# Optimization experiments

Measured on AMD Instinct MI355X. Metric: run time of the kernel, lower is better.

## Reference

```python
import jax, jax.numpy as jnp
import numpy as np

B, L, IN, H, W = 4096, 10, 8, 512, 512


def setup_inputs() -> dict:
    key = jax.random.key(0)
    ks = jax.random.split(key, 24)
    s = 0.05  # small init so tanh/sigmoid stay in active range
    def rn(k, shape):
        return jax.random.normal(k, shape, dtype=jnp.float32) * s
    return {
        "items": jax.random.normal(ks[0], (B, L, IN), dtype=jnp.float32),
        "decoder_items_input": jax.random.uniform(ks[1], (B, H), dtype=jnp.float32),
        "emb_w": rn(ks[2], (H, IN)), "emb_b": rn(ks[3], (H,)),
        "enc_wih": rn(ks[4], (3 * H, H)), "enc_whh": rn(ks[5], (3 * H, H)),
        "enc_bih": rn(ks[6], (3 * H,)), "enc_bhh": rn(ks[7], (3 * H,)),
        "dec_wih": rn(ks[8], (3 * H, H)), "dec_whh": rn(ks[9], (3 * H, H)),
        "dec_bih": rn(ks[10], (3 * H,)), "dec_bhh": rn(ks[11], (3 * H,)),
        "w1": rn(ks[12], (W, H)), "w2": rn(ks[13], (W, H)),
        "w3": rn(ks[14], (W, H)), "w4": rn(ks[15], (W, H)),
        "w5": rn(ks[16], (W, H)), "w6": rn(ks[17], (W, H)),
        "w7": rn(ks[18], (W, 2 * H)),
        "v1": rn(ks[19], (W,)), "v2": rn(ks[20], (W,)),
        "v3_w": rn(ks[21], (W,)), "v3_b": rn(ks[22], (1,)),
        "wori": rn(ks[23], (6, 3 * H)), "bori": jnp.zeros((6,), jnp.float32),
    }


def _gru_scan(xg, whh, bhh, h0):
    # xg: [L,B,3H] precomputed input-gate projections; returns all hidden states [L,B,H]
    def step(h, xg_t):
        hg = h @ whh.T + bhh
        xr, xz, xn = jnp.split(xg_t, 3, axis=-1)
        hr, hz, hn = jnp.split(hg, 3, axis=-1)
        r = jax.nn.sigmoid(xr + hr)
        z = jax.nn.sigmoid(xz + hz)
        n = jnp.tanh(xn + r * hn)
        h_new = (1.0 - z) * n + z * h
        return h_new, h_new
    _, ys = jax.lax.scan(step, h0, xg)
    return ys


def _forward(items, decoder_items_input, emb_w, emb_b, enc_wih, enc_whh, enc_bih, enc_bhh,
             dec_wih, dec_whh, dec_bih, dec_bhh, w1, w2, w3, w4, w5, w6, w7,
             v1, v2, v3_w, v3_b, wori, bori):
    Bsz, Lln, _ = items.shape
    Hh = emb_w.shape[0]
    x = items @ emb_w.T + emb_b                                  # [B,L,H] embedding
    xg = (x @ enc_wih.T + enc_bih).transpose(1, 0, 2)            # [L,B,3H]
    enc_out = _gru_scan(xg, enc_whh, enc_bhh, jnp.zeros((Bsz, Hh), x.dtype))  # [L,B,H]
    h0 = enc_out[-1]                                             # last encoder state
    enc_blh = enc_out.transpose(1, 0, 2)                         # [B,L,H]
    enc_w3 = enc_out @ w3.T                                      # [L,B,W] (hoisted, step-invariant)
    enc_w6 = enc_out @ w6.T                                      # [L,B,W]
    xg_dec = decoder_items_input @ dec_wih.T + dec_bih           # [B,3H] constant decoder input
    xr, xz, xn = jnp.split(xg_dec, 3, axis=-1)

    def step(h, _):
        hg = h @ dec_whh.T + dec_bhh
        hr, hz, hn = jnp.split(hg, 3, axis=-1)
        r = jax.nn.sigmoid(xr + hr)
        z = jax.nn.sigmoid(xz + hz)
        n = jnp.tanh(xn + r * hn)
        h_new = (1.0 - z) * n + z * h                            # GRUCell update
        # intra attention cache is always length-1 in the source (the shape[1]==1 branch
        # always fires), so log_softmax is over a singleton axis -> exactly zero.
        doi = h_new[:, None, :]                                  # [B,1,H]
        oi = jnp.tanh(h_new @ w1.T + h_new @ w2.T) @ v1          # [B]
        attnd = jax.nn.log_softmax(oi[:, None, None], axis=-1)   # [B,1,1] zeros
        hi = (attnd * doi).sum(axis=1)                           # [B,H] (zeros, faithful)
        sm = jnp.tanh(enc_w3 + h_new @ w4.T + hi @ w5.T)         # [L,B,W]
        out_seq = (sm @ v2).T                                    # [B,L]
        sm_ori = jnp.tanh(enc_w6 + jnp.concatenate([h_new, hi], axis=-1) @ w7.T)  # [L,B,W]
        oo = sm_ori @ v3_w + v3_b[0]                             # [L,B]
        attnc = jax.nn.log_softmax(oo.T[:, :, None], axis=-1)    # [B,L,1] zeros (singleton axis)
        he = (attnc * enc_blh).sum(axis=1)                       # [B,H]
        total = jnp.concatenate([he, h_new, hi], axis=-1)        # [B,3H]
        out_ori = total @ wori.T + bori                          # [B,6]
        return h_new, (out_seq, out_ori)

    _, (seqs, oris) = jax.lax.scan(step, h0, None, length=Lln)
    probs_seq = seqs.transpose(1, 0, 2)                          # [B,L,L]
    probs_ori = oris.transpose(1, 0, 2)                          # [B,L,6]
    return probs_seq, probs_ori


def reference(items, decoder_items_input, emb_w, emb_b, enc_wih, enc_whh, enc_bih, enc_bhh,
              dec_wih, dec_whh, dec_bih, dec_bhh, w1, w2, w3, w4, w5, w6, w7,
              v1, v2, v3_w, v3_b, wori, bori):
    return _forward(items, decoder_items_input, emb_w, emb_b, enc_wih, enc_whh, enc_bih,
                    enc_bhh, dec_wih, dec_whh, dec_bih, dec_bhh, w1, w2, w3, w4, w5, w6,
                    w7, v1, v2, v3_w, v3_b, wori, bori)
```

## Files before the change

kernel.cpp:

```cpp
#include <hip/hip_runtime.h>
#include <hip/hip_bf16.h>


#define B_   4096
#define L_   10
#define IN_  8
#define H_   512
#define H3_  1536
#define W_   512
#define ORI_BASE (B_ * L_ * L_)

typedef __attribute__((ext_vector_type(8))) short s8v;
typedef __attribute__((ext_vector_type(4))) float f4v;

#define LOG2E  1.4426950408889634f
#define LOG2E2 2.8853900817779268f

__device__ __forceinline__ float sig_fast(float x) {
  float e = __builtin_amdgcn_exp2f(-x * LOG2E);
  return __builtin_amdgcn_rcpf(1.f + e);
}
__device__ __forceinline__ float tanh_fast(float x) {
  float e = __builtin_amdgcn_exp2f(x * LOG2E2);
  return 1.f - 2.f * __builtin_amdgcn_rcpf(e + 1.f);
}
__device__ __forceinline__ short f2bf(float f) {
  __hip_bfloat16 h = __float2bfloat16(f);
  return __builtin_bit_cast(short, h);
}
__device__ __forceinline__ float bf2f(short s) {
  __hip_bfloat16 h = __builtin_bit_cast(__hip_bfloat16, s);
  return __bfloat162float(h);
}
__device__ __forceinline__ void stc(float* p, float v) { *p = v; }
__device__ __forceinline__ void stc(short* p, float v) { *p = f2bf(v); }

__global__ __launch_bounds__(256) void f2bf_k(const float* __restrict__ src,
                                              short* __restrict__ dst, int n)
{
  int i = blockIdx.x * 256 + threadIdx.x;
  if (i < n) dst[i] = f2bf(src[i]);
}

__global__ __launch_bounds__(256) void build_wc(
    const float* __restrict__ enc_wih, const float* __restrict__ emb_w,
    const float* __restrict__ emb_b, const float* __restrict__ enc_bih,
    float* __restrict__ Wc, float* __restrict__ bc)
{
  __shared__ float se[H_ * IN_];
  __shared__ float sb[H_];
  const int tid = threadIdx.x;
  for (int i = tid; i < H_ * IN_; i += 256) se[i] = emb_w[i];
  for (int i = tid; i < H_; i += 256) sb[i] = emb_b[i];
  __syncthreads();
  int g = (blockIdx.x * 256 + tid) >> 6;
  int lane = tid & 63;
  const float* wr = enc_wih + (long)g * H_ + lane * 8;
  float w8[8];
#pragma unroll
  for (int j = 0; j < 8; ++j) w8[j] = wr[j];
  float acc[9] = {};
#pragma unroll
  for (int kk = 0; kk < 8; ++kk) {
    int k = lane * 8 + kk;
#pragma unroll
    for (int j = 0; j < 8; ++j) acc[j] += w8[kk] * se[k * IN_ + j];
    acc[8] += w8[kk] * sb[k];
  }
#pragma unroll
  for (int j = 0; j < 9; ++j)
#pragma unroll
    for (int off = 32; off; off >>= 1) acc[j] += __shfl_down(acc[j], off, 64);
  if (lane == 0) {
#pragma unroll
    for (int j = 0; j < 8; ++j) Wc[g * IN_ + j] = acc[j];
    bc[g] = acc[8] + enc_bih[g];
  }
}

template <typename CT>
__global__ __launch_bounds__(256) void gemm_bf16(
    const short* __restrict__ A, long lda,
    const short* __restrict__ Bw, long ldb,
    const float* __restrict__ bias,
    CT* __restrict__ C, long ldc, int K, float scale)
{
  __shared__ short As[128 * 32];
  __shared__ short Bs[128 * 32];
  const int tid = threadIdx.x;
  const long row0 = (long)blockIdx.y * 128;
  const long col0 = (long)blockIdx.x * 128;
  const int wave = tid >> 6, lane = tid & 63;
  const int wm = (wave & 1) * 64, wn = (wave >> 1) * 64;
  const int r16 = lane & 15, quad = lane >> 4;
  f4v acc[4][4] = {};

  for (int k0 = 0; k0 < K; k0 += 32) {
#pragma unroll
    for (int r = 0; r < 2; ++r) {
      int idx = r * 256 + tid;
      int m = idx >> 2;
      int k8 = (idx & 3) * 8;
      __builtin_amdgcn_global_load_lds(
          (const __attribute__((address_space(1))) void*)(A + (row0 + m) * lda + k0 + k8),
          (__attribute__((address_space(3))) void*)(As + idx * 8), 16, 0, 0);
      __builtin_amdgcn_global_load_lds(
          (const __attribute__((address_space(1))) void*)(Bw + (col0 + m) * ldb + k0 + k8),
          (__attribute__((address_space(3))) void*)(Bs + idx * 8), 16, 0, 0);
    }
    __syncthreads();
    s8v af[4], bf[4];
#pragma unroll
    for (int i = 0; i < 4; ++i)
      af[i] = *(const s8v*)&As[(wm + i * 16 + r16) * 32 + quad * 8];
#pragma unroll
    for (int j = 0; j < 4; ++j)
      bf[j] = *(const s8v*)&Bs[(wn + j * 16 + r16) * 32 + quad * 8];
#pragma unroll
    for (int i = 0; i < 4; ++i)
#pragma unroll
      for (int j = 0; j < 4; ++j)
        acc[i][j] = __builtin_amdgcn_mfma_f32_16x16x32_bf16(af[i], bf[j], acc[i][j], 0, 0, 0);
    __syncthreads();
  }

#pragma unroll
  for (int i = 0; i < 4; ++i) {
    long rbase = row0 + wm + i * 16 + quad * 4;
#pragma unroll
    for (int j = 0; j < 4; ++j) {
      long c = col0 + wn + j * 16 + r16;
      float bv = bias ? bias[c] : 0.f;
#pragma unroll
      for (int rg = 0; rg < 4; ++rg)
        stc(&C[(rbase + rg) * ldc + c], (acc[i][j][rg] + bv) * scale);
    }
  }
}

template <bool ENC>
__global__ __launch_bounds__(256) void gru_fused(
    const short* __restrict__ Aprev,
    const short* __restrict__ Whh,
    const float* __restrict__ bhh,
    const short* __restrict__ xg,
    const float* __restrict__ items_t,
    const float* __restrict__ Wc,
    const float* __restrict__ bc,
    float* __restrict__ h,
    short* __restrict__ hout)
{
  __shared__ short As[2][64 * 64];
  __shared__ short Bs[2][192 * 64];
  const int tid = threadIdx.x;
  const long row0 = (long)blockIdx.y * 64;
  const int col0 = blockIdx.x * 64;
  const int wave = tid >> 6, lane = tid & 63;
  const int r16 = lane & 15, quad = lane >> 4;
  const int sw = r16 & 7;

  f4v acc[3][4] = {};

  auto stage = [&](int buf, int k0) {
#pragma unroll
    for (int r = 0; r < 2; ++r) {
      int idx = r * 256 + tid;
      int m = idx >> 3, c8 = idx & 7;
      int src = c8 ^ (m & 7);
      __builtin_amdgcn_global_load_lds(
          (const __attribute__((address_space(1))) void*)(Aprev + (row0 + m) * H_ + k0 + src * 8),
          (__attribute__((address_space(3))) void*)(&As[buf][idx * 8]), 16, 0, 0);
    }
#pragma unroll
    for (int r = 0; r < 6; ++r) {
      int idx = r * 256 + tid;
      int m = idx >> 3, c8 = idx & 7;
      int src = c8 ^ (m & 7);
      int g = m >> 6, cc = m & 63;
      __builtin_amdgcn_global_load_lds(
          (const __attribute__((address_space(1))) void*)(Whh + ((long)g * H_ + col0 + cc) * H_ + k0 + src * 8),
          (__attribute__((address_space(3))) void*)(&Bs[buf][idx * 8]), 16, 0, 0);
    }
  };

  stage(0, 0);
  int cur = 0;
  for (int k = 0; k < 8; ++k) {
    if (k < 7) {
      stage(cur ^ 1, (k + 1) * 64);
      asm volatile("s_waitcnt vmcnt(8)" ::: "memory");
    } else {
      asm volatile("s_waitcnt vmcnt(0)" ::: "memory");
    }
    __builtin_amdgcn_s_barrier();
    s8v af[4][2], bf[3][2];
#pragma unroll
    for (int i = 0; i < 4; ++i)
#pragma unroll
      for (int hh = 0; hh < 2; ++hh)
        af[i][hh] = *(const s8v*)&As[cur][(i * 16 + r16) * 64 + ((hh * 4 + quad) ^ sw) * 8];
#pragma unroll
    for (int g = 0; g < 3; ++g)
#pragma unroll
      for (int hh = 0; hh < 2; ++hh)
        bf[g][hh] = *(const s8v*)&Bs[cur][(g * 64 + wave * 16 + r16) * 64 + ((hh * 4 + quad) ^ sw) * 8];
    __builtin_amdgcn_s_setprio(1);
#pragma unroll
    for (int hh = 0; hh < 2; ++hh)
#pragma unroll
      for (int g = 0; g < 3; ++g)
#pragma unroll
        for (int i = 0; i < 4; ++i)
          acc[g][i] = __builtin_amdgcn_mfma_f32_16x16x32_bf16(af[i][hh], bf[g][hh], acc[g][i], 0, 0, 0);
    __builtin_amdgcn_s_setprio(0);
    __builtin_amdgcn_s_barrier();
    cur ^= 1;
  }

  const int col = col0 + wave * 16 + r16;
  float wc[3][8], bcv[3];
  if (ENC) {
#pragma unroll
    for (int g = 0; g < 3; ++g) {
      const float* wr = Wc + ((long)g * H_ + col) * IN_;
#pragma unroll
      for (int j = 0; j < 8; ++j) wc[g][j] = wr[j];
      bcv[g] = bc[g * H_ + col];
    }
    float* itemS = (float*)As;
    int i2 = tid * 2;
    int m = i2 >> 3, j = i2 & 7;
    itemS[i2] = items_t[(row0 + m) * (L_ * IN_) + j];
    itemS[i2 + 1] = items_t[(row0 + m) * (L_ * IN_) + j + 1];
    __syncthreads();
  }
  float bhr = bhh[col], bhz = bhh[col + H_], bhn = bhh[col + 2 * H_];

#pragma unroll
  for (int i = 0; i < 4; ++i) {
#pragma unroll
    for (int rg = 0; rg < 4; ++rg) {
      int rl = i * 16 + quad * 4 + rg;
      long row = row0 + rl;
      float xr, xz, xn;
      if (ENC) {
        const float* it = (const float*)As + rl * 8;
        xr = bcv[0]; xz = bcv[1]; xn = bcv[2];
#pragma unroll
        for (int j = 0; j < 8; ++j) {
          float iv = it[j];
          xr += iv * wc[0][j];
          xz += iv * wc[1][j];
          xn += iv * wc[2][j];
        }
      } else {
        long gx = row * H3_ + col;
        xr = bf2f(xg[gx]); xz = bf2f(xg[gx + H_]); xn = bf2f(xg[gx + 2 * H_]);
      }
      float r = sig_fast(xr + acc[0][i][rg] + bhr);
      float z = sig_fast(xz + acc[1][i][rg] + bhz);
      float n = tanh_fast(xn + r * (acc[2][i][rg] + bhn));
      long hi = row * H_ + col;
      float hv = (1.f - z) * n + z * h[hi];
      h[hi] = hv;
      hout[hi] = f2bf(hv);
    }
  }
}

__global__ __launch_bounds__(256) void out_seq_all(
    const short* __restrict__ ew3,
    const short* __restrict__ a4,
    const float* __restrict__ v2,
    float* __restrict__ out)
{
  __shared__ float se[L_ * W_];
  __shared__ float sa[L_ * W_];
  const int b = blockIdx.x;
  const int tid = threadIdx.x;
  for (int i = tid; i < L_ * W_ / 8; i += 256) {
    int l = i >> 6, c = i & 63;
    s8v ev = *(const s8v*)(ew3 + ((long)l * B_ + b) * W_ + c * 8);
    s8v av = *(const s8v*)(a4 + ((long)l * B_ + b) * W_ + c * 8);
    f4v e0, e1, a0, a1;
#pragma unroll
    for (int j = 0; j < 4; ++j) {
      e0[j] = bf2f(ev[j]); e1[j] = bf2f(ev[j + 4]);
      a0[j] = bf2f(av[j]); a1[j] = bf2f(av[j + 4]);
    }
    *(f4v*)(se + i * 8) = e0; *(f4v*)(se + i * 8 + 4) = e1;
    *(f4v*)(sa + i * 8) = a0; *(f4v*)(sa + i * 8 + 4) = a1;
  }
  const int wave = tid >> 6, lane = tid & 63;
  float svp[8], svtot = 0.f;
#pragma unroll
  for (int j = 0; j < 8; ++j) {
    float v = v2[lane * 8 + j];
    svp[j] = -2.f * v;
    svtot += v;
  }
#pragma unroll
  for (int off = 32; off; off >>= 1) svtot += __shfl_down(svtot, off, 64);
  __syncthreads();

#pragma unroll
  for (int pp = 0; pp < 25; ++pp) {
    int p = wave * 25 + pp;
    int t = p / L_, l = p - t * L_;
    const float* ep = se + l * W_ + lane * 8;
    const float* ap = sa + t * W_ + lane * 8;
    f4v e0 = *(const f4v*)ep, e1 = *(const f4v*)(ep + 4);
    f4v a0 = *(const f4v*)ap, a1 = *(const f4v*)(ap + 4);
    float acc = 0.f;
#pragma unroll
    for (int j = 0; j < 4; ++j) {
      float x0 = __builtin_amdgcn_exp2f(e0[j] + a0[j]);
      acc += svp[j] * __builtin_amdgcn_rcpf(x0 + 1.f);
      float x1 = __builtin_amdgcn_exp2f(e1[j] + a1[j]);
      acc += svp[j + 4] * __builtin_amdgcn_rcpf(x1 + 1.f);
    }
#pragma unroll
    for (int off = 32; off; off >>= 1) acc += __shfl_down(acc, off, 64);
    if (lane == 0) out[((long)b * L_ + t) * L_ + l] = svtot + acc;
  }
}

__global__ __launch_bounds__(256) void out_ori_all(
    const short* __restrict__ dh,
    const float* __restrict__ wori, const float* __restrict__ bori,
    float* __restrict__ out)
{
  int wid = (blockIdx.x * 256 + threadIdx.x) >> 6;
  int lane = threadIdx.x & 63;
  int b = wid / L_, t = wid - b * L_;
  s8v hv = *(const s8v*)(dh + ((long)t * B_ + b) * H_ + lane * 8);
  float hf[8];
#pragma unroll
  for (int j = 0; j < 8; ++j) hf[j] = bf2f(hv[j]);
  float res[6];
#pragma unroll
  for (int o = 0; o < 6; ++o) {
    const float* wr = wori + (long)o * H3_ + H_ + lane * 8;
    float acc = 0.f;
#pragma unroll
    for (int j = 0; j < 8; ++j) acc += hf[j] * wr[j];
#pragma unroll
    for (int off = 32; off; off >>= 1) acc += __shfl_down(acc, off, 64);
    res[o] = acc;
  }
  if (lane == 0) {
    float* po = out + ORI_BASE + ((long)b * L_ + t) * 6;
#pragma unroll
    for (int o = 0; o < 6; ++o) po[o] = res[o] + bori[o];
  }
}

extern "C" void kernel_launch(void* const* d_in, const int* in_sizes, int n_in,
                              void* d_out, int out_size, void* d_ws, size_t ws_size,
                              hipStream_t stream)
{
  const float* items   = (const float*)d_in[0];
  const float* dec_in  = (const float*)d_in[1];
  const float* emb_w   = (const float*)d_in[2];
  const float* emb_b   = (const float*)d_in[3];
  const float* enc_wih = (const float*)d_in[4];
  const float* enc_whh = (const float*)d_in[5];
  const float* enc_bih = (const float*)d_in[6];
  const float* enc_bhh = (const float*)d_in[7];
  const float* dec_wih = (const float*)d_in[8];
  const float* dec_whh = (const float*)d_in[9];
  const float* dec_bih = (const float*)d_in[10];
  const float* dec_bhh = (const float*)d_in[11];
  const float* w3      = (const float*)d_in[14];
  const float* w4      = (const float*)d_in[15];
  const float* v2      = (const float*)d_in[20];
  const float* wori    = (const float*)d_in[23];
  const float* bori    = (const float*)d_in[24];
  float* out = (float*)d_out;

  char* ws = (char*)d_ws;
  size_t off = 0;
  auto alloc = [&](size_t bytes) { size_t o = off; off += (bytes + 255) & ~255UL; return o; };
  float* Wc       = (float*)(ws + alloc(H3_ * IN_ * 4));
  float* bc       = (float*)(ws + alloc(H3_ * 4));
  float* h        = (float*)(ws + alloc((size_t)B_ * H_ * 4));
  short* xgb      = (short*)(ws + alloc((size_t)B_ * H3_ * 2));
  short* enc_hist = (short*)(ws + alloc((size_t)11 * B_ * H_ * 2));
  short* dec_hist = (short*)(ws + alloc((size_t)L_ * B_ * H_ * 2));
  short* ew3      = (short*)(ws + alloc((size_t)L_ * B_ * W_ * 2));
  short* a4       = (short*)(ws + alloc((size_t)L_ * B_ * W_ * 2));
  short* whh_e    = (short*)(ws + alloc((size_t)H3_ * H_ * 2));
  short* whh_d    = (short*)(ws + alloc((size_t)H3_ * H_ * 2));
  short* wih_d    = (short*)(ws + alloc((size_t)H3_ * H_ * 2));
  short* w3b      = (short*)(ws + alloc((size_t)W_ * H_ * 2));
  short* w4b      = (short*)(ws + alloc((size_t)W_ * H_ * 2));
  short* decb     = (short*)(ws + alloc((size_t)B_ * H_ * 2));

  f2bf_k<<<(H3_ * H_ + 255) / 256, 256, 0, stream>>>(enc_whh, whh_e, H3_ * H_);
  f2bf_k<<<(H3_ * H_ + 255) / 256, 256, 0, stream>>>(dec_whh, whh_d, H3_ * H_);
  f2bf_k<<<(H3_ * H_ + 255) / 256, 256, 0, stream>>>(dec_wih, wih_d, H3_ * H_);
  f2bf_k<<<(W_ * H_ + 255) / 256, 256, 0, stream>>>(w3, w3b, W_ * H_);
  f2bf_k<<<(W_ * H_ + 255) / 256, 256, 0, stream>>>(w4, w4b, W_ * H_);
  f2bf_k<<<(B_ * H_ + 255) / 256, 256, 0, stream>>>(dec_in, decb, B_ * H_);
  build_wc<<<384, 256, 0, stream>>>(enc_wih, emb_w, emb_b, enc_bih, Wc, bc);

  hipMemsetAsync(h, 0, (size_t)B_ * H_ * 4, stream);
  hipMemsetAsync(enc_hist, 0, (size_t)B_ * H_ * 2, stream);

  for (int t = 0; t < L_; ++t) {
    gru_fused<true><<<dim3(8, 64), 256, 0, stream>>>(
        enc_hist + (size_t)t * B_ * H_, whh_e, enc_bhh, nullptr,
        items + (size_t)t * IN_, Wc, bc, h,
        enc_hist + (size_t)(t + 1) * B_ * H_);
  }

  gemm_bf16<short><<<dim3(12, 32), 256, 0, stream>>>(
      decb, H_, wih_d, H_, dec_bih, xgb, H3_, H_, 1.f);

  for (int t = 0; t < L_; ++t) {
    const short* prev = (t == 0) ? enc_hist + (size_t)10 * B_ * H_
                                 : dec_hist + (size_t)(t - 1) * B_ * H_;
    gru_fused<false><<<dim3(8, 64), 256, 0, stream>>>(
        prev, whh_d, dec_bhh, xgb, nullptr, nullptr, nullptr, h,
        dec_hist + (size_t)t * B_ * H_);
  }

  gemm_bf16<short><<<dim3(4, 320), 256, 0, stream>>>(
      enc_hist + (size_t)B_ * H_, H_, w3b, H_, nullptr, ew3, W_, H_, LOG2E2);
  gemm_bf16<short><<<dim3(4, 320), 256, 0, stream>>>(
      dec_hist, H_, w4b, H_, nullptr, a4, W_, H_, LOG2E2);
  out_seq_all<<<B_, 256, 0, stream>>>(ew3, a4, v2, out);
  out_ori_all<<<(B_ * L_) / 4, 256, 0, stream>>>(dec_hist, wori, bori, out);
}
```

Measured before the change: 632.4 us.

## Fuse encoder and decoder GRU steps into one persistent kernel with row-group barriers

Result: slower. 1.029 ms (+62.7%).

```diff
diff --git a/kernel.cpp b/kernel.cpp
--- a/kernel.cpp
+++ b/kernel.cpp
@@ -11,6 +11,7 @@
 #define ORI_BASE (B_ * L_ * L_)
 
 typedef __attribute__((ext_vector_type(8))) short s8v;
+typedef __attribute__((ext_vector_type(4))) short s4v;
 typedef __attribute__((ext_vector_type(4))) float f4v;
 
 #define LOG2E  1.4426950408889634f
@@ -138,132 +139,193 @@
   }
 }
 
-template <bool ENC>
-__global__ __launch_bounds__(256) void gru_fused(
-    const short* __restrict__ Aprev,
-    const short* __restrict__ Whh,
-    const float* __restrict__ bhh,
-    const short* __restrict__ xg,
-    const float* __restrict__ items_t,
-    const float* __restrict__ Wc,
-    const float* __restrict__ bc,
-    float* __restrict__ h,
-    short* __restrict__ hout)
-{
-  __shared__ short As[2][64 * 64];
-  __shared__ short Bs[2][192 * 64];
+__global__ __launch_bounds__(512, 2) void gru_chain(
+    const short* __restrict__ whh_e, const float* __restrict__ bhh_e,
+    const short* __restrict__ whh_d, const float* __restrict__ bhh_d,
+    const short* __restrict__ xgb,
+    const float* __restrict__ items,
+    const float* __restrict__ Wc, const float* __restrict__ bc,
+    short* __restrict__ enc_hist,
+    short* __restrict__ dec_hist,
+    unsigned* __restrict__ bar)
+{
+  extern __shared__ short smem[];
+  short* AsB = smem;
+  short* BsB = smem + 16384;
   const int tid = threadIdx.x;
-  const long row0 = (long)blockIdx.y * 64;
-  const int col0 = blockIdx.x * 64;
+  const int f = blockIdx.x;
+  const int by = (f & 7) * 4 + (f >> 6);
+  const int bx = (f >> 3) & 7;
+  const long row0 = (long)by * 128;
+  const int col0 = bx * 64;
   const int wave = tid >> 6, lane = tid & 63;
+  const int rw = wave & 1, cw = wave >> 1;
   const int r16 = lane & 15, quad = lane >> 4;
   const int sw = r16 & 7;
-
-  f4v acc[3][4] = {};
-
-  auto stage = [&](int buf, int k0) {
+  const int col = col0 + cw * 16 + r16;
+
+  float hreg[16] = {};
+  f4v acc[3][4];
+
+  auto stage = [&](const short* Ap, const short* Whh, int buf, int k0) {
 #pragma unroll
     for (int r = 0; r < 2; ++r) {
-      int idx = r * 256 + tid;
+      int idx = r * 512 + tid;
       int m = idx >> 3, c8 = idx & 7;
       int src = c8 ^ (m & 7);
       __builtin_amdgcn_global_load_lds(
-          (const __attribute__((address_space(1))) void*)(Aprev + (row0 + m) * H_ + k0 + src * 8),
-          (__attribute__((address_space(3))) void*)(&As[buf][idx * 8]), 16, 0, 0);
-    }
-#pragma unroll
-    for (int r = 0; r < 6; ++r) {
-      int idx = r * 256 + tid;
+          (const __attribute__((address_space(1))) void*)(Ap + (row0 + m) * H_ + k0 + src * 8),
+          (__attribute__((address_space(3))) void*)(AsB + buf * 8192 + idx * 8), 16, 0, 0);
+    }
+#pragma unroll
+    for (int r = 0; r < 3; ++r) {
+      int idx = r * 512 + tid;
       int m = idx >> 3, c8 = idx & 7;
       int src = c8 ^ (m & 7);
       int g = m >> 6, cc = m & 63;
       __builtin_amdgcn_global_load_lds(
           (const __attribute__((address_space(1))) void*)(Whh + ((long)g * H_ + col0 + cc) * H_ + k0 + src * 8),
-          (__attribute__((address_space(3))) void*)(&Bs[buf][idx * 8]), 16, 0, 0);
+          (__attribute__((address_space(3))) void*)(BsB + buf * 12288 + idx * 8), 16, 0, 0);
     }
   };
 
-  stage(0, 0);
-  int cur = 0;
-  for (int k = 0; k < 8; ++k) {
-    if (k < 7) {
-      stage(cur ^ 1, (k + 1) * 64);
-      asm volatile("s_waitcnt vmcnt(8)" ::: "memory");
-    } else {
-      asm volatile("s_waitcnt vmcnt(0)" ::: "memory");
-    }
-    __builtin_amdgcn_s_barrier();
-    s8v af[4][2], bf[3][2];
-#pragma unroll
-    for (int i = 0; i < 4; ++i)
+  auto kloop = [&](const short* Ap, const short* Whh) {
+#pragma unroll
+    for (int g = 0; g < 3; ++g)
+#pragma unroll
+      for (int i = 0; i < 4; ++i) acc[g][i] = (f4v){0.f, 0.f, 0.f, 0.f};
+    stage(Ap, Whh, 0, 0);
+    for (int k = 0; k < 8; ++k) {
+      if (k < 7) {
+        stage(Ap, Whh, (k + 1) & 1, (k + 1) * 64);
+        asm volatile("s_waitcnt vmcnt(5)" ::: "memory");
+      } else {
+        asm volatile("s_waitcnt vmcnt(0)" ::: "memory");
+      }
+      __builtin_amdgcn_s_barrier();
+      const short* Asc = AsB + (k & 1) * 8192;
+      const short* Bsc = BsB + (k & 1) * 12288;
+      s8v af[4][2], bf[3][2];
+#pragma unroll
+      for (int i = 0; i < 4; ++i)
+#pragma unroll
+        for (int hh = 0; hh < 2; ++hh)
+          af[i][hh] = *(const s8v*)&Asc[(rw * 64 + i * 16 + r16) * 64 + ((hh * 4 + quad) ^ sw) * 8];
+#pragma unroll
+      for (int g = 0; g < 3; ++g)
+#pragma unroll
+        for (int hh = 0; hh < 2; ++hh)
+          bf[g][hh] = *(const s8v*)&Bsc[(g * 64 + cw * 16 + r16) * 64 + ((hh * 4 + quad) ^ sw) * 8];
+      __builtin_amdgcn_s_setprio(1);
 #pragma unroll
       for (int hh = 0; hh < 2; ++hh)
-        af[i][hh] = *(const s8v*)&As[cur][(i * 16 + r16) * 64 + ((hh * 4 + quad) ^ sw) * 8];
-#pragma unroll
-    for (int g = 0; g < 3; ++g)
-#pragma unroll
-      for (int hh = 0; hh < 2; ++hh)
-        bf[g][hh] = *(const s8v*)&Bs[cur][(g * 64 + wave * 16 + r16) * 64 + ((hh * 4 + quad) ^ sw) * 8];
-    __builtin_amdgcn_s_setprio(1);
-#pragma unroll
-    for (int hh = 0; hh < 2; ++hh)
+#pragma unroll
+        for (int g = 0; g < 3; ++g)
+#pragma unroll
+          for (int i = 0; i < 4; ++i)
+            acc[g][i] = __builtin_amdgcn_mfma_f32_16x16x32_bf16(af[i][hh], bf[g][hh], acc[g][i], 0, 0, 0);
+      __builtin_amdgcn_s_setprio(0);
+      __builtin_amdgcn_s_barrier();
+    }
+  };
+
+  unsigned step = 0;
+  auto gsync = [&]() {
+    ++step;
+    __syncthreads();
+    if (tid == 0) {
+      __threadfence();
+      __hip_atomic_fetch_add(&bar[by], 1u, __ATOMIC_RELEASE, __HIP_MEMORY_SCOPE_AGENT);
+      unsigned tgt = 8u * step;
+      while (__hip_atomic_load(&bar[by], __ATOMIC_ACQUIRE, __HIP_MEMORY_SCOPE_AGENT) < tgt)
+        __builtin_amdgcn_s_sleep(2);
+      __threadfence();
+    }
+    __syncthreads();
+  };
+
+  float wc[3][8], bcv[3];
+#pragma unroll
+  for (int g = 0; g < 3; ++g) {
+    const float* wr = Wc + ((long)g * H_ + col) * IN_;
+#pragma unroll
+    for (int j = 0; j < 8; ++j) wc[g][j] = wr[j];
+    bcv[g] = bc[g * H_ + col];
+  }
+  {
+    float bhr = bhh_e[col], bhz = bhh_e[col + H_], bhn = bhh_e[col + 2 * H_];
+    for (int t = 0; t < L_; ++t) {
+      kloop(enc_hist + (size_t)t * B_ * H_, whh_e);
+      float* itemS = (float*)AsB;
+      const float* items_t = items + (size_t)t * IN_;
+      {
+        int i2 = tid * 2;
+        int m = i2 >> 3, j = i2 & 7;
+        itemS[i2] = items_t[(row0 + m) * (L_ * IN_) + j];
+        itemS[i2 + 1] = items_t[(row0 + m) * (L_ * IN_) + j + 1];
+      }
+      __syncthreads();
+      short* hout = enc_hist + (size_t)(t + 1) * B_ * H_;
+#pragma unroll
+      for (int i = 0; i < 4; ++i) {
+#pragma unroll
+        for (int rg = 0; rg < 4; ++rg) {
+          int rl = rw * 64 + i * 16 + quad * 4 + rg;
+          long row = row0 + rl;
+          const float* it = itemS + rl * 8;
+          float xr = bcv[0], xz = bcv[1], xn = bcv[2];
+#pragma unroll
+          for (int j = 0; j < 8; ++j) {
+            float iv = it[j];
+            xr += iv * wc[0][j];
+            xz += iv * wc[1][j];
+            xn += iv * wc[2][j];
+          }
+          float r = sig_fast(xr + acc[0][i][rg] + bhr);
+          float z = sig_fast(xz + acc[1][i][rg] + bhz);
+          float n = tanh_fast(xn + r * (acc[2][i][rg] + bhn));
+          int hx = i * 4 + rg;
+          float hv = (1.f - z) * n + z * hreg[hx];
+          hreg[hx] = hv;
+          hout[row * H_ + col] = f2bf(hv);
+        }
+      }
+      gsync();
+    }
+  }
+
+  float xv[3][16];
+#pragma unroll
+  for (int i = 0; i < 4; ++i)
+#pragma unroll
+    for (int rg = 0; rg < 4; ++rg) {
+      long row = row0 + rw * 64 + i * 16 + quad * 4 + rg;
 #pragma unroll
       for (int g = 0; g < 3; ++g)
-#pragma unroll
-        for (int i = 0; i < 4; ++i)
-          acc[g][i] = __builtin_amdgcn_mfma_f32_16x16x32_bf16(af[i][hh], bf[g][hh], acc[g][i], 0, 0, 0);
-    __builtin_amdgcn_s_setprio(0);
-    __builtin_amdgcn_s_barrier();
-    cur ^= 1;
-  }
-
-  const int col = col0 + wave * 16 + r16;
-  float wc[3][8], bcv[3];
-  if (ENC) {
-#pragma unroll
-    for (int g = 0; g < 3; ++g) {
-      const float* wr = Wc + ((long)g * H_ + col) * IN_;
-#pragma unroll
-      for (int j = 0; j < 8; ++j) wc[g][j] = wr[j];
-      bcv[g] = bc[g * H_ + col];
-    }
-    float* itemS = (float*)As;
-    int i2 = tid * 2;
-    int m = i2 >> 3, j = i2 & 7;
-    itemS[i2] = items_t[(row0 + m) * (L_ * IN_) + j];
-    itemS[i2 + 1] = items_t[(row0 + m) * (L_ * IN_) + j + 1];
-    __syncthreads();
-  }
-  float bhr = bhh[col], bhz = bhh[col + H_], bhn = bhh[col + 2 * H_];
-
-#pragma unroll
-  for (int i = 0; i < 4; ++i) {
-#pragma unroll
-    for (int rg = 0; rg < 4; ++rg) {
-      int rl = i * 16 + quad * 4 + rg;
-      long row = row0 + rl;
-      float xr, xz, xn;
-      if (ENC) {
-        const float* it = (const float*)As + rl * 8;
-        xr = bcv[0]; xz = bcv[1]; xn = bcv[2];
-#pragma unroll
-        for (int j = 0; j < 8; ++j) {
-          float iv = it[j];
-          xr += iv * wc[0][j];
-          xz += iv * wc[1][j];
-          xn += iv * wc[2][j];
+        xv[g][i * 4 + rg] = bf2f(xgb[row * H3_ + g * H_ + col]);
+    }
+  {
+    float bhr = bhh_d[col], bhz = bhh_d[col + H_], bhn = bhh_d[col + 2 * H_];
+    for (int t = 0; t < L_; ++t) {
+      const short* Ap = (t == 0) ? enc_hist + (size_t)10 * B_ * H_
+                                 : dec_hist + (size_t)(t - 1) * B_ * H_;
+      kloop(Ap, whh_d);
+      short* hout = dec_hist + (size_t)t * B_ * H_;
+#pragma unroll
+      for (int i = 0; i < 4; ++i) {
+#pragma unroll
+        for (int rg = 0; rg < 4; ++rg) {
+          int hx = i * 4 + rg;
+          long row = row0 + rw * 64 + i * 16 + quad * 4 + rg;
+          float r = sig_fast(xv[0][hx] + acc[0][i][rg] + bhr);
+          float z = sig_fast(xv[1][hx] + acc[1][i][rg] + bhz);
+          float n = tanh_fast(xv[2][hx] + r * (acc[2][i][rg] + bhn));
+          float hv = (1.f - z) * n + z * hreg[hx];
+          hreg[hx] = hv;
+          hout[row * H_ + col] = f2bf(hv);
         }
-      } else {
-        long gx = row * H3_ + col;
-        xr = bf2f(xg[gx]); xz = bf2f(xg[gx + H_]); xn = bf2f(xg[gx + 2 * H_]);
       }
-      float r = sig_fast(xr + acc[0][i][rg] + bhr);
-      float z = sig_fast(xz + acc[1][i][rg] + bhz);
-      float n = tanh_fast(xn + r * (acc[2][i][rg] + bhn));
-      long hi = row * H_ + col;
-      float hv = (1.f - z) * n + z * h[hi];
-      h[hi] = hv;
-      hout[hi] = f2bf(hv);
+      if (t < L_ - 1) gsync();
     }
   }
 }
@@ -278,46 +340,50 @@
   __shared__ float sa[L_ * W_];
   const int b = blockIdx.x;
   const int tid = threadIdx.x;
-  for (int i = tid; i < L_ * W_ / 8; i += 256) {
-    int l = i >> 6, c = i & 63;
-    s8v ev = *(const s8v*)(ew3 + ((long)l * B_ + b) * W_ + c * 8);
-    s8v av = *(const s8v*)(a4 + ((long)l * B_ + b) * W_ + c * 8);
-    f4v e0, e1, a0, a1;
-#pragma unroll
-    for (int j = 0; j < 4; ++j) {
-      e0[j] = bf2f(ev[j]); e1[j] = bf2f(ev[j + 4]);
-      a0[j] = bf2f(av[j]); a1[j] = bf2f(av[j + 4]);
-    }
-    *(f4v*)(se + i * 8) = e0; *(f4v*)(se + i * 8 + 4) = e1;
-    *(f4v*)(sa + i * 8) = a0; *(f4v*)(sa + i * 8 + 4) = a1;
+  for (int i = tid; i < L_ * 128; i += 256) {
+    int row = i >> 7, q = i & 127;
+    s4v ev = *(const s4v*)(ew3 + ((long)row * B_ + b) * W_ + q * 4);
+    s4v av = *(const s4v*)(a4 + ((long)row * B_ + b) * W_ + q * 4);
+    f4v e, a;
+#pragma unroll
+    for (int j = 0; j < 4; ++j) { e[j] = bf2f(ev[j]); a[j] = bf2f(av[j]); }
+    *(f4v*)(se + row * W_ + q * 4) = e;
+    *(f4v*)(sa + row * W_ + q * 4) = a;
   }
   const int wave = tid >> 6, lane = tid & 63;
-  float svp[8], svtot = 0.f;
-#pragma unroll
-  for (int j = 0; j < 8; ++j) {
-    float v = v2[lane * 8 + j];
-    svp[j] = -2.f * v;
-    svtot += v;
+  float sv0[4], sv1[4], svtot = 0.f;
+#pragma unroll
+  for (int q = 0; q < 4; ++q) {
+    float v = v2[lane * 4 + q];
+    sv0[q] = -2.f * v; svtot += v;
+    v = v2[256 + lane * 4 + q];
+    sv1[q] = -2.f * v; svtot += v;
   }
 #pragma unroll
   for (int off = 32; off; off >>= 1) svtot += __shfl_down(svtot, off, 64);
+  svtot = __shfl(svtot, 0, 64);
   __syncthreads();
 
+  int tprev = -1;
+  f4v a0, a1;
 #pragma unroll
   for (int pp = 0; pp < 25; ++pp) {
     int p = wave * 25 + pp;
     int t = p / L_, l = p - t * L_;
-    const float* ep = se + l * W_ + lane * 8;
-    const float* ap = sa + t * W_ + lane * 8;
-    f4v e0 = *(const f4v*)ep, e1 = *(const f4v*)(ep + 4);
-    f4v a0 = *(const f4v*)ap, a1 = *(const f4v*)(ap + 4);
+    if (t != tprev) {
+      a0 = *(const f4v*)(sa + t * W_ + lane * 4);
+      a1 = *(const f4v*)(sa + t * W_ + 256 + lane * 4);
+      tprev = t;
+    }
+    f4v e0 = *(const f4v*)(se + l * W_ + lane * 4);
+    f4v e1 = *(const f4v*)(se + l * W_ + 256 + lane * 4);
     float acc = 0.f;
 #pragma unroll
-    for (int j = 0; j < 4; ++j) {
-      float x0 = __builtin_amdgcn_exp2f(e0[j] + a0[j]);
-      acc += svp[j] * __builtin_amdgcn_rcpf(x0 + 1.f);
-      float x1 = __builtin_amdgcn_exp2f(e1[j] + a1[j]);
-      acc += svp[j + 4] * __builtin_amdgcn_rcpf(x1 + 1.f);
+    for (int q = 0; q < 4; ++q) {
+      float x0 = __builtin_amdgcn_exp2f(e0[q] + a0[q]);
+      acc += sv0[q] * __builtin_amdgcn_rcpf(x0 + 1.f);
+      float x1 = __builtin_amdgcn_exp2f(e1[q] + a1[q]);
+      acc += sv1[q] * __builtin_amdgcn_rcpf(x1 + 1.f);
     }
 #pragma unroll
     for (int off = 32; off; off >>= 1) acc += __shfl_down(acc, off, 64);
@@ -383,7 +449,7 @@
   auto alloc = [&](size_t bytes) { size_t o = off; off += (bytes + 255) & ~255UL; return o; };
   float* Wc       = (float*)(ws + alloc(H3_ * IN_ * 4));
   float* bc       = (float*)(ws + alloc(H3_ * 4));
-  float* h        = (float*)(ws + alloc((size_t)B_ * H_ * 4));
+  unsigned* bar   = (unsigned*)(ws + alloc(32 * 4));
   short* xgb      = (short*)(ws + alloc((size_t)B_ * H3_ * 2));
   short* enc_hist = (short*)(ws + alloc((size_t)11 * B_ * H_ * 2));
   short* dec_hist = (short*)(ws + alloc((size_t)L_ * B_ * H_ * 2));
@@ -404,26 +470,21 @@
   f2bf_k<<<(B_ * H_ + 255) / 256, 256, 0, stream>>>(dec_in, decb, B_ * H_);
   build_wc<<<384, 256, 0, stream>>>(enc_wih, emb_w, emb_b, enc_bih, Wc, bc);
 
-  hipMemsetAsync(h, 0, (size_t)B_ * H_ * 4, stream);
   hipMemsetAsync(enc_hist, 0, (size_t)B_ * H_ * 2, stream);
-
-  for (int t = 0; t < L_; ++t) {
-    gru_fused<true><<<dim3(8, 64), 256, 0, stream>>>(
-        enc_hist + (size_t)t * B_ * H_, whh_e, enc_bhh, nullptr,
-        items + (size_t)t * IN_, Wc, bc, h,
-        enc_hist + (size_t)(t + 1) * B_ * H_);
-  }
+  hipMemsetAsync(bar, 0, 32 * 4, stream);
 
   gemm_bf16<short><<<dim3(12, 32), 256, 0, stream>>>(
       decb, H_, wih_d, H_, dec_bih, xgb, H3_, H_, 1.f);
 
-  for (int t = 0; t < L_; ++t) {
-    const short* prev = (t == 0) ? enc_hist + (size_t)10 * B_ * H_
-                                 : dec_hist + (size_t)(t - 1) * B_ * H_;
-    gru_fused<false><<<dim3(8, 64), 256, 0, stream>>>(
-        prev, whh_d, dec_bhh, xgb, nullptr, nullptr, nullptr, h,
-        dec_hist + (size_t)t * B_ * H_);
-  }
+  static bool attr_set = false;
+  if (!attr_set) {
+    (void)hipFuncSetAttribute((const void*)gru_chain,
+                              hipFuncAttributeMaxDynamicSharedMemorySize, 81920);
+    attr_set = true;
+  }
+  gru_chain<<<256, 512, 81920, stream>>>(
+      whh_e, enc_bhh, whh_d, dec_bhh, xgb, items, Wc, bc,
+      enc_hist, dec_hist, bar);
 
   gemm_bf16<short><<<dim3(4, 320), 256, 0, stream>>>(
       enc_hist + (size_t)B_ * H_, H_, w3b, H_, nullptr, ew3, W_, H_, LOG2E2);
```
